# Kernel optimization log

Hardware: AMD Instinct MI355X
Metric: run time of the kernel (lower is better)

The kernel has to match this reference:

```python
import jax, jax.numpy as jnp
import numpy as np

B, DM, H, D, N = 1024, 512, 8, 64, 81  # batch, d_model, nhead, depth, tokens (9x9)


def setup_inputs() -> dict:
    key = jax.random.key(0)
    k1, k2, k3, k4, k5 = jax.random.split(key, 5)
    return {
        "x": jax.random.normal(k1, (B, DM, 9, 9), dtype=jnp.float32),
        "qkv_w": jax.random.normal(k2, (3 * DM, DM), dtype=jnp.float32) * 0.02,
        "qkv_b": jax.random.normal(k3, (3 * DM,), dtype=jnp.float32) * 0.02,
        "rel_h": jax.random.normal(k4, (1, H, D, 1, 9), dtype=jnp.float32),
        "rel_w": jax.random.normal(k5, (1, H, D, 9, 1), dtype=jnp.float32),
    }


def reference(x, qkv_w, qkv_b, rel_h, rel_w):
    b = x.shape[0]
    xf = x.reshape(b, DM, N)                                   # [B, C, 81]
    # 1x1 conv == channel matmul
    qkv = jnp.einsum('oc,bcn->bon', qkv_w, xf) + qkv_b[None, :, None]
    q, k, v = jnp.split(qkv, 3, axis=1)                         # each [B, DM, 81]
    q = q.reshape(b, H, D, N).transpose(0, 1, 3, 2)             # [B, H, 81, D]
    k = k.reshape(b, H, D, N)                                   # [B, H, D, 81]
    v = v.reshape(b, H, D, N).transpose(0, 1, 3, 2)             # [B, H, 81, D]
    content_content = jnp.einsum('bhnd,bhdm->bhnm', q, k)       # [B, H, 81, 81]
    r = (rel_h + rel_w).reshape(H, D, N)                        # broadcast add -> [H, D, 81]
    content_position = jnp.einsum('bhnd,hdm->bhnm', q, r)       # [B, H, 81, 81]
    attention = jax.nn.softmax(content_content + content_position, axis=-1)
    out = jnp.einsum('bhnm,bhmd->bhnd', attention, v)            # [B, H, 81, D]
    return out.transpose(0, 1, 3, 2).reshape(b, DM, 9, 9)
```

## Files before the change

### kernel.cpp

```cpp
#include <hip/hip_runtime.h>
#include <hip/hip_bf16.h>
#include <cstdint>
#include <cstddef>

#define NB 1024
#define DM 512
#define NH 8
#define HD 64
#define NT 81
#define O3 1536
#define NP 96

typedef __bf16 bf16x8 __attribute__((ext_vector_type(8)));
typedef float  f32x4  __attribute__((ext_vector_type(4)));
typedef unsigned short us8 __attribute__((ext_vector_type(8)));

__device__ __forceinline__ unsigned short f2bf(float f) {
    unsigned u = __builtin_bit_cast(unsigned, f);
    u += 0x7fffu + ((u >> 16) & 1u);
    return (unsigned short)(u >> 16);
}
__device__ __forceinline__ float bf2f(unsigned short h) {
    unsigned u = ((unsigned)h) << 16;
    return __builtin_bit_cast(float, u);
}
__device__ __forceinline__ bf16x8 ld8(const unsigned short* p) {
    return __builtin_bit_cast(bf16x8, *(const us8*)p);
}
__device__ __forceinline__ void async16(void* lds, const void* g) {
    __builtin_amdgcn_global_load_lds(
        (const __attribute__((address_space(1))) void*)g,
        (__attribute__((address_space(3))) void*)lds, 16, 0, 0);
}

__global__ void conv_w(const float* __restrict__ w, unsigned short* __restrict__ wb, int n) {
    int i = blockIdx.x * 256 + threadIdx.x;
    if (i < n) wb[i] = f2bf(w[i]);
}

__global__ __launch_bounds__(256) void transpose_x(
    const float* __restrict__ x, unsigned short* __restrict__ xT)
{
    __shared__ float sT[64][85];
    const int tid = threadIdx.x;
    const int b  = blockIdx.x >> 3;
    const int c0 = (blockIdx.x & 7) * 64;
    const float* xb = x + ((size_t)b * DM + c0) * NT;

    const int nn = tid & 31, cc0 = tid >> 5;
    for (int i = 0; i < 8; ++i) {
        int cc = cc0 + i * 8;
        const float* xr = xb + (size_t)cc * NT;
        #pragma unroll
        for (int j = 0; j < 3; ++j) {
            int n = nn + 32 * j;
            if (n < NT) sT[cc][n] = xr[n];
        }
    }
    __syncthreads();

    const int ci = tid & 7, n0 = tid >> 3;
    for (int i = 0; i < 3; ++i) {
        int n = n0 + 32 * i;
        us8 v;
        #pragma unroll
        for (int j = 0; j < 8; ++j) {
            float f = (n < NT) ? sT[ci * 8 + j][n] : 0.f;
            v[j] = f2bf(f);
        }
        *(us8*)(xT + ((size_t)b * NP + n) * DM + c0 + ci * 8) = v;
    }
}

#define OT 256
#define KC 32

__global__ __launch_bounds__(256) void qkv_gemm_a(
    const unsigned short* __restrict__ xT,
    const unsigned short* __restrict__ wb,
    const float* __restrict__ bias,
    const float* __restrict__ relh,
    const float* __restrict__ relw,
    unsigned short* __restrict__ qkv)
{
    __shared__ __align__(16) unsigned short sW[OT * KC];
    __shared__ __align__(16) unsigned short sX[NP * KC];

    const int tid  = threadIdx.x;
    const int lane = tid & 63;
    const int wv   = tid >> 6;
    const int b    = blockIdx.x / 6;
    const int ot   = blockIdx.x % 6;
    const int o0   = ot * OT;
    const int r16  = lane & 15;
    const int q8   = (lane >> 4) * 8;

    f32x4 acc[4][6];
    #pragma unroll
    for (int i = 0; i < 4; ++i)
        #pragma unroll
        for (int j = 0; j < 6; ++j)
            acc[i][j] = (f32x4){0.f, 0.f, 0.f, 0.f};

    const unsigned short* xb = xT + (size_t)b * NP * DM;

    for (int kc = 0; kc < DM; kc += KC) {
        #pragma unroll
        for (int i = 0; i < 4; ++i) {
            int ch  = i * 256 + wv * 64 + lane;
            int row = ch >> 2, cb = ch & 3;
            async16(&sW[(i * 256 + wv * 64) * 8],
                    wb + (size_t)(o0 + row) * DM + kc + cb * 8);
        }
        {
            int ch  = wv * 64 + lane;
            int row = ch >> 2, cb = ch & 3;
            async16(&sX[(wv * 64) * 8], xb + (size_t)row * DM + kc + cb * 8);
            if (wv < 2) {
                int ch2  = 256 + wv * 64 + lane;
                int row2 = ch2 >> 2, cb2 = ch2 & 3;
                async16(&sX[(256 + wv * 64) * 8], xb + (size_t)row2 * DM + kc + cb2 * 8);
            }
        }
        __syncthreads();
        bf16x8 af[4], bfr[6];
        #pragma unroll
        for (int i = 0; i < 4; ++i)
            af[i] = ld8(&sW[(wv * 64 + i * 16 + r16) * KC + q8]);
        #pragma unroll
        for (int nt = 0; nt < 6; ++nt)
            bfr[nt] = ld8(&sX[(nt * 16 + r16) * KC + q8]);
        #pragma unroll
        for (int i = 0; i < 4; ++i)
            #pragma unroll
            for (int nt = 0; nt < 6; ++nt)
                acc[i][nt] = __builtin_amdgcn_mfma_f32_16x16x32_bf16(af[i], bfr[nt], acc[i][nt], 0, 0, 0);
        __syncthreads();
    }

    unsigned short* qb = qkv + (size_t)b * O3 * NT;
    #pragma unroll
    for (int i = 0; i < 4; ++i) {
        int obase = o0 + (wv * 4 + i) * 16 + (lane >> 4) * 4;
        #pragma unroll
        for (int nt = 0; nt < 6; ++nt) {
            int n = nt * 16 + r16;
            if (n < NT) {
                #pragma unroll
                for (int r = 0; r < 4; ++r) {
                    int o = obase + r;
                    float v = acc[i][nt][r] + bias[o];
                    if (o >= DM && o < 2 * DM) {
                        int oo = o - DM;
                        v += relh[oo * 9 + (n % 9)] + relw[oo * 9 + (n / 9)];
                    }
                    qb[(size_t)o * NT + n] = f2bf(v);
                }
            }
        }
    }
}

#define OTILE 128
#define SWS 40
#define SXS 40

__global__ __launch_bounds__(256) void qkv_gemm_fb(
    const float* __restrict__ x,
    const unsigned short* __restrict__ wb,
    const float* __restrict__ bias,
    const float* __restrict__ relh,
    const float* __restrict__ relw,
    unsigned short* __restrict__ qkv)
{
    __shared__ unsigned short sW[OTILE * SWS];
    __shared__ unsigned short sXT[NP * SXS];

    const int tid  = threadIdx.x;
    const int lane = tid & 63;
    const int wv   = tid >> 6;
    const int b    = blockIdx.x / (O3 / OTILE);
    const int ot   = blockIdx.x % (O3 / OTILE);
    const int o0   = ot * OTILE;
    const int r16 = lane & 15;
    const int q8  = (lane >> 4) * 8;

    f32x4 acc[2][6];
    for (int i = 0; i < 2; ++i)
        for (int j = 0; j < 6; ++j)
            acc[i][j] = (f32x4){0.f, 0.f, 0.f, 0.f};

    const float* xb = x + (size_t)b * DM * NT;
    const int wr  = tid >> 2;
    const int wc  = (tid & 3) * 8;
    const int xc  = tid >> 3;
    const int xn0 = tid & 7;

    for (int kc = 0; kc < DM; kc += 32) {
        {
            us8 v0 = *(const us8*)(wb + (size_t)(o0 + wr) * DM + kc + wc);
            us8 v1 = *(const us8*)(wb + (size_t)(o0 + wr + 64) * DM + kc + wc);
            *(us8*)(&sW[wr * SWS + wc]) = v0;
            *(us8*)(&sW[(wr + 64) * SWS + wc]) = v1;
        }
        {
            const float* xr = xb + (size_t)(kc + xc) * NT;
            #pragma unroll
            for (int j = 0; j < 12; ++j) {
                int n = xn0 + 8 * j;
                float v = (n < NT) ? xr[n] : 0.f;
                sXT[n * SXS + xc] = f2bf(v);
            }
        }
        __syncthreads();
        bf16x8 af0 = ld8(&sW[((wv * 2 + 0) * 16 + r16) * SWS + q8]);
        bf16x8 af1 = ld8(&sW[((wv * 2 + 1) * 16 + r16) * SWS + q8]);
        #pragma unroll
        for (int nt = 0; nt < 6; ++nt) {
            bf16x8 bfr = ld8(&sXT[(nt * 16 + r16) * SXS + q8]);
            acc[0][nt] = __builtin_amdgcn_mfma_f32_16x16x32_bf16(af0, bfr, acc[0][nt], 0, 0, 0);
            acc[1][nt] = __builtin_amdgcn_mfma_f32_16x16x32_bf16(af1, bfr, acc[1][nt], 0, 0, 0);
        }
        __syncthreads();
    }

    unsigned short* qb = qkv + (size_t)b * O3 * NT;
    #pragma unroll
    for (int i = 0; i < 2; ++i) {
        int obase = o0 + (wv * 2 + i) * 16 + (lane >> 4) * 4;
        #pragma unroll
        for (int nt = 0; nt < 6; ++nt) {
            int n = nt * 16 + r16;
            if (n < NT) {
                #pragma unroll
                for (int r = 0; r < 4; ++r) {
                    int o = obase + r;
                    float v = acc[i][nt][r] + bias[o];
                    if (o >= DM && o < 2 * DM) {
                        int oo = o - DM;
                        v += relh[oo * 9 + (n % 9)] + relw[oo * 9 + (n / 9)];
                    }
                    qb[(size_t)o * NT + n] = f2bf(v);
                }
            }
        }
    }
}

#define SQS 72
#define SPS 104
#define SVS 104

__global__ __launch_bounds__(384, 6) void attn(
    const unsigned short* __restrict__ qkv,
    float* __restrict__ out)
{
    __shared__ __align__(16) unsigned short smem[20480];
    unsigned short* sQ   = smem;
    unsigned short* sK   = smem + 96 * SQS;
    unsigned short* sP   = smem;
    float*          sRcp = (float*)(smem + 96 * SPS);
    unsigned short* sV   = smem + 2 * 96 * SQS;

    const int tid  = threadIdx.x;
    const int lane = tid & 63;
    const int wv   = tid >> 6;
    const int c    = lane & 15;
    const int q    = lane >> 4;
    const int q8   = q * 8;
    const int b    = blockIdx.x >> 3;
    const int h    = blockIdx.x & 7;

    const unsigned short* qp = qkv + (size_t)b * O3 * NT + (size_t)(h * HD) * NT;
    const unsigned short* kp = qp + (size_t)DM * NT;
    const unsigned short* vp = qp + (size_t)(2 * DM) * NT;

    {
        const int n   = tid % 96;
        const int d2b = tid / 96;
        #pragma unroll
        for (int i = 0; i < 8; ++i) {
            int d2 = d2b * 8 + i;
            unsigned q0 = 0, q1 = 0, k0 = 0, k1 = 0;
            if (n < NT) {
                q0 = qp[(2 * d2) * NT + n]; q1 = qp[(2 * d2 + 1) * NT + n];
                k0 = kp[(2 * d2) * NT + n]; k1 = kp[(2 * d2 + 1) * NT + n];
            }
            ((unsigned*)sQ)[n * 36 + d2] = q0 | (q1 << 16);
            ((unsigned*)sK)[n * 36 + d2] = k0 | (k1 << 16);
        }
    }
    for (int idx = tid; idx < HD * 52; idx += 384) {
        int d = idx / 52, m2 = idx - d * 52;
        int m0 = 2 * m2;
        unsigned e0 = (m0 < NT)     ? (unsigned)vp[d * NT + m0]     : 0u;
        unsigned e1 = (m0 + 1 < NT) ? (unsigned)vp[d * NT + m0 + 1] : 0u;
        ((unsigned*)sV)[d * 52 + m2] = e0 | (e1 << 16);
    }
    __syncthreads();

    f32x4 acc[6];
    #pragma unroll
    for (int mt = 0; mt < 6; ++mt) acc[mt] = (f32x4){0.f, 0.f, 0.f, 0.f};
    #pragma unroll
    for (int kk = 0; kk < 2; ++kk) {
        bf16x8 qa = ld8(&sQ[(wv * 16 + c) * SQS + kk * 32 + q8]);
        #pragma unroll
        for (int mt = 0; mt < 6; ++mt) {
            bf16x8 kb = ld8(&sK[(mt * 16 + c) * SQS + kk * 32 + q8]);
            acc[mt] = __builtin_amdgcn_mfma_f32_16x16x32_bf16(qa, kb, acc[mt], 0, 0, 0);
        }
    }
    #pragma unroll
    for (int r = 0; r < 4; ++r)
        acc[5][r] = (c == 0) ? acc[5][r] : -3.0e38f;

    float rcp[4];
    #pragma unroll
    for (int r = 0; r < 4; ++r) {
        float mx = fmaxf(fmaxf(fmaxf(acc[0][r], acc[1][r]), fmaxf(acc[2][r], acc[3][r])),
                         fmaxf(acc[4][r], acc[5][r]));
        mx = fmaxf(mx, __shfl_xor(mx, 1));
        mx = fmaxf(mx, __shfl_xor(mx, 2));
        mx = fmaxf(mx, __shfl_xor(mx, 4));
        mx = fmaxf(mx, __shfl_xor(mx, 8));
        float s = 0.f;
        #pragma unroll
        for (int mt = 0; mt < 6; ++mt) {
            float e = exp2f((acc[mt][r] - mx) * 1.44269504088896f);
            acc[mt][r] = e;
            s += bf2f(f2bf(e));
        }
        s += __shfl_xor(s, 1);
        s += __shfl_xor(s, 2);
        s += __shfl_xor(s, 4);
        s += __shfl_xor(s, 8);
        rcp[r] = 1.0f / s;
    }

    __syncthreads();

    #pragma unroll
    for (int mt = 0; mt < 6; ++mt)
        #pragma unroll
        for (int r = 0; r < 4; ++r)
            sP[(wv * 16 + 4 * q + r) * SPS + mt * 16 + c] = f2bf(acc[mt][r]);
    if (c == 0) {
        #pragma unroll
        for (int r = 0; r < 4; ++r)
            sRcp[wv * 16 + 4 * q + r] = rcp[r];
    }

    f32x4 oacc[4];
    #pragma unroll
    for (int dt = 0; dt < 4; ++dt) oacc[dt] = (f32x4){0.f, 0.f, 0.f, 0.f};
    #pragma unroll
    for (int kt = 0; kt < 3; ++kt) {
        bf16x8 pb = ld8(&sP[(wv * 16 + c) * SPS + kt * 32 + q8]);
        #pragma unroll
        for (int dt = 0; dt < 4; ++dt) {
            bf16x8 va = ld8(&sV[(dt * 16 + c) * SVS + kt * 32 + q8]);
            oacc[dt] = __builtin_amdgcn_mfma_f32_16x16x32_bf16(va, pb, oacc[dt], 0, 0, 0);
        }
    }

    float* ob = out + (size_t)b * DM * NT + (size_t)(h * HD) * NT;
    const int n = wv * 16 + c;
    if (n < NT) {
        float rs = sRcp[n];
        #pragma unroll
        for (int dt = 0; dt < 4; ++dt) {
            #pragma unroll
            for (int r = 0; r < 4; ++r)
                ob[(size_t)(dt * 16 + 4 * q + r) * NT + n] = oacc[dt][r] * rs;
        }
    }
}

extern "C" void kernel_launch(void* const* d_in, const int* in_sizes, int n_in,
                              void* d_out, int out_size, void* d_ws, size_t ws_size,
                              hipStream_t stream) {
    const float* x     = (const float*)d_in[0];
    const float* qkv_w = (const float*)d_in[1];
    const float* qkv_b = (const float*)d_in[2];
    const float* rel_h = (const float*)d_in[3];
    const float* rel_w = (const float*)d_in[4];
    float* out = (float*)d_out;

    unsigned short* qkv = (unsigned short*)d_ws;
    unsigned short* wb  = qkv + (size_t)NB * O3 * NT;
    unsigned short* xT  = wb + (size_t)O3 * DM;
    size_t need = ((size_t)NB * O3 * NT + (size_t)O3 * DM + (size_t)NB * NP * DM) * 2;

    conv_w<<<dim3((O3 * DM + 255) / 256), dim3(256), 0, stream>>>(qkv_w, wb, O3 * DM);
    if (ws_size >= need) {
        transpose_x<<<dim3(NB * 8), dim3(256), 0, stream>>>(x, xT);
        qkv_gemm_a<<<dim3(NB * 6), dim3(256), 0, stream>>>(xT, wb, qkv_b, rel_h, rel_w, qkv);
    } else {
        qkv_gemm_fb<<<dim3(NB * 12), dim3(256), 0, stream>>>(x, wb, qkv_b, rel_h, rel_w, qkv);
    }
    attn<<<dim3(NB * NH), dim3(384), 0, stream>>>(qkv, out);
}
```

Baseline: 810.3 us.

## Double-buffer QKV GEMM shared tiles with XOR swizzle and occupancy hint

Splits the QKV projection GEMM's shared-memory tiles into two buffers so the async global-to-LDS copy of the next K chunk overlaps with MFMA compute on the current one, removing one barrier per step. It also XOR-swizzles the 16-byte column chunks by row to reduce LDS bank conflicts on the fragment loads, and adds a min-blocks-per-CU launch bound of 3. The cost is double the LDS footprint and tighter register pressure from the occupancy hint. The loop is hard-coded to 16 K steps, so it depends on DM/KC staying fixed.

```diff
diff --git a/kernel.cpp b/kernel.cpp
--- a/kernel.cpp
+++ b/kernel.cpp
@@ -75,7 +75,7 @@
 #define OT 256
 #define KC 32
 
-__global__ __launch_bounds__(256) void qkv_gemm_a(
+__global__ __launch_bounds__(256, 3) void qkv_gemm_a(
     const unsigned short* __restrict__ xT,
     const unsigned short* __restrict__ wb,
     const float* __restrict__ bias,
@@ -83,8 +83,8 @@
     const float* __restrict__ relw,
     unsigned short* __restrict__ qkv)
 {
-    __shared__ __align__(16) unsigned short sW[OT * KC];
-    __shared__ __align__(16) unsigned short sX[NP * KC];
+    __shared__ __align__(16) unsigned short sW[2][OT * KC];
+    __shared__ __align__(16) unsigned short sX[2][NP * KC];
 
     const int tid  = threadIdx.x;
     const int lane = tid & 63;
@@ -94,6 +94,7 @@
     const int o0   = ot * OT;
     const int r16  = lane & 15;
     const int q8   = (lane >> 4) * 8;
+    const int sq8  = q8 ^ ((r16 & 3) * 8);
 
     f32x4 acc[4][6];
     #pragma unroll
@@ -104,37 +105,54 @@
 
     const unsigned short* xb = xT + (size_t)b * NP * DM;
 
-    for (int kc = 0; kc < DM; kc += KC) {
+    auto stage = [&](int bi, int kc) {
+        unsigned short* dW = &sW[bi][0];
+        unsigned short* dX = &sX[bi][0];
         #pragma unroll
         for (int i = 0; i < 4; ++i) {
             int ch  = i * 256 + wv * 64 + lane;
             int row = ch >> 2, cb = ch & 3;
-            async16(&sW[(i * 256 + wv * 64) * 8],
-                    wb + (size_t)(o0 + row) * DM + kc + cb * 8);
+            int cbs = cb ^ (row & 3);
+            async16(dW + (i * 256 + wv * 64) * 8,
+                    wb + (size_t)(o0 + row) * DM + kc + cbs * 8);
         }
         {
             int ch  = wv * 64 + lane;
             int row = ch >> 2, cb = ch & 3;
-            async16(&sX[(wv * 64) * 8], xb + (size_t)row * DM + kc + cb * 8);
+            int cbs = cb ^ (row & 3);
+            async16(dX + (wv * 64) * 8, xb + (size_t)row * DM + kc + cbs * 8);
             if (wv < 2) {
                 int ch2  = 256 + wv * 64 + lane;
                 int row2 = ch2 >> 2, cb2 = ch2 & 3;
-                async16(&sX[(256 + wv * 64) * 8], xb + (size_t)row2 * DM + kc + cb2 * 8);
+                int cbs2 = cb2 ^ (row2 & 3);
+                async16(dX + (256 + wv * 64) * 8, xb + (size_t)row2 * DM + kc + cbs2 * 8);
             }
         }
-        __syncthreads();
+    };
+
+    auto compute = [&](const unsigned short* bW, const unsigned short* bX) {
         bf16x8 af[4], bfr[6];
         #pragma unroll
         for (int i = 0; i < 4; ++i)
-            af[i] = ld8(&sW[(wv * 64 + i * 16 + r16) * KC + q8]);
+            af[i] = ld8(&bW[(wv * 64 + i * 16 + r16) * KC + sq8]);
         #pragma unroll
         for (int nt = 0; nt < 6; ++nt)
-            bfr[nt] = ld8(&sX[(nt * 16 + r16) * KC + q8]);
+            bfr[nt] = ld8(&bX[(nt * 16 + r16) * KC + sq8]);
         #pragma unroll
         for (int i = 0; i < 4; ++i)
             #pragma unroll
             for (int nt = 0; nt < 6; ++nt)
                 acc[i][nt] = __builtin_amdgcn_mfma_f32_16x16x32_bf16(af[i], bfr[nt], acc[i][nt], 0, 0, 0);
+    };
+
+    stage(0, 0);
+    __syncthreads();
+    for (int ks = 0; ks < 16; ks += 2) {
+        stage(1, (ks + 1) * KC);
+        compute(&sW[0][0], &sX[0][0]);
+        __syncthreads();
+        if (ks + 2 < 16) stage(0, (ks + 2) * KC);
+        compute(&sW[1][0], &sX[1][0]);
         __syncthreads();
     }
 
```

Result: faster. 759.6 us (-6.3%).
